# Performance work log

Hardware: AMD Instinct MI355X
Metric: run time of the kernel (lower is better)

## Reference

```python
import jax, jax.numpy as jnp
import numpy as np

IN_F = 4096
OUT_F = 4096
R = 16
LORA_ALPHA = 32
SCALING = LORA_ALPHA / R  # 2.0


def setup_inputs() -> dict:
    key = jax.random.key(0)
    k_x, k_w, k_b, k_a, k_bb = jax.random.split(key, 5)
    x = jax.random.normal(k_x, (4, 2048, IN_F), dtype=jnp.float32)
    # Simulate _quantize_4bit: build a float weight, quantize per-row to int4.
    w = jax.random.normal(k_w, (OUT_F, IN_F), dtype=jnp.float32) * 0.02
    max_abs = jnp.clip(jnp.max(jnp.abs(w), axis=1, keepdims=True), 1e-8, None)
    qscale = max_abs / 7.0                                   # [OUT_F, 1] float32
    qweight = jnp.clip(jnp.round(w / qscale), -8, 7).astype(jnp.int32)  # [OUT_F, IN_F]
    bias = jax.random.normal(k_b, (OUT_F,), dtype=jnp.float32) * 0.01
    # LoRA: A kaiming-uniform-like, B random (zeros init would make the LoRA path trivially zero).
    bound = 1.0 / np.sqrt(IN_F)
    lora_A = jax.random.uniform(k_a, (R, IN_F), minval=-bound, maxval=bound, dtype=jnp.float32)
    lora_B = jax.random.normal(k_bb, (OUT_F, R), dtype=jnp.float32) * 0.01
    return {"x": x, "qweight": qweight, "qscale": qscale, "bias": bias,
            "lora_A": lora_A, "lora_B": lora_B}


def reference(x, qweight, qscale, bias, lora_A, lora_B):
    # Dequantize int4 weights with per-row scale: W[o, i] = q[o, i] * s[o]
    W = qweight.astype(x.dtype) * qscale.astype(x.dtype)     # [OUT_F, IN_F]
    base = jnp.einsum('bsi,oi->bso', x, W) + bias            # F.linear(x, W, bias)
    # LoRA low-rank path (dropout=0 -> identity)
    lora = jnp.einsum('bsr,or->bso', jnp.einsum('bsi,ri->bsr', x, lora_A), lora_B)
    return base + lora * SCALING
```

## Files before the change

kernel.cpp:

```cpp
#include <hip/hip_runtime.h>
#include <hip/hip_bf16.h>
#include <stdint.h>


#define IN_F 4096
#define OUT_F 4096

typedef unsigned short u16;
typedef __attribute__((ext_vector_type(8))) short s16x8;
typedef __attribute__((ext_vector_type(4))) float f32x4;

__device__ inline u16 f2bf(float f) {
    union { float f; uint32_t u; } v; v.f = f;
    uint32_t u = v.u;
    return (u16)((u + 0x7FFFu + ((u >> 16) & 1u)) >> 16);
}

__global__ __launch_bounds__(256) void cvt_x_kernel(const float* __restrict__ x,
                                                    u16* __restrict__ xb, int n8) {
    int t = blockIdx.x * 256 + threadIdx.x;
    if (t >= n8) return;
    const float4* src = (const float4*)x + (size_t)t * 2;
    float4 a = src[0], b = src[1];
    union { u16 u[8]; s16x8 v; } o;
    o.u[0] = f2bf(a.x); o.u[1] = f2bf(a.y); o.u[2] = f2bf(a.z); o.u[3] = f2bf(a.w);
    o.u[4] = f2bf(b.x); o.u[5] = f2bf(b.y); o.u[6] = f2bf(b.z); o.u[7] = f2bf(b.w);
    ((s16x8*)xb)[t] = o.v;
}

__global__ __launch_bounds__(256) void build_weff_kernel(const int* __restrict__ qw,
                                                         const float* __restrict__ qs,
                                                         const float* __restrict__ lA,
                                                         const float* __restrict__ lB,
                                                         u16* __restrict__ w) {
    int t = blockIdx.x * 256 + threadIdx.x;
    int o  = t >> 9;
    int i0 = (t & 511) << 3;
    float s = qs[o];
    const int4* q4 = (const int4*)(qw + (size_t)o * IN_F + i0);
    int4 qa = q4[0], qb = q4[1];
    float acc[8];
    acc[0] = qa.x * s; acc[1] = qa.y * s; acc[2] = qa.z * s; acc[3] = qa.w * s;
    acc[4] = qb.x * s; acc[5] = qb.y * s; acc[6] = qb.z * s; acc[7] = qb.w * s;
#pragma unroll
    for (int r = 0; r < 16; ++r) {
        float br = 2.0f * lB[o * 16 + r];
        const float4* a4 = (const float4*)(lA + (size_t)r * IN_F + i0);
        float4 aa = a4[0], ab = a4[1];
        acc[0] += br * aa.x; acc[1] += br * aa.y; acc[2] += br * aa.z; acc[3] += br * aa.w;
        acc[4] += br * ab.x; acc[5] += br * ab.y; acc[6] += br * ab.z; acc[7] += br * ab.w;
    }
    union { u16 u[8]; s16x8 v; } ov;
#pragma unroll
    for (int j = 0; j < 8; ++j) ov.u[j] = f2bf(acc[j]);
    ((s16x8*)w)[t] = ov.v;
}

#define BK 32
#define NT (IN_F / BK)

#define GLD16(gp, lp)                                                          \
    __builtin_amdgcn_global_load_lds(                                          \
        (const __attribute__((address_space(1))) void*)(gp),                   \
        (__attribute__((address_space(3))) void*)(lp), 16, 0, 0)

__global__ __launch_bounds__(512, 2) void gemm_bt_kernel(const short* __restrict__ Xb,
                                                         const short* __restrict__ Wb,
                                                         const float* __restrict__ bias,
                                                         float* __restrict__ out,
                                                         int nmt) {
    __shared__ __align__(16) char smem[131072];

    const int tid  = threadIdx.x;
    const int w    = tid >> 6, lane = tid & 63;
    const int wm   = w >> 2, wn = w & 3;
    const int rl   = lane & 15;

    const int nwg = nmt * 16;
    const int cpx = nwg >> 3;
    const int f   = blockIdx.x;
    const int swz = (f & 7) * cpx + (f >> 3);
    const int m0  = (swz >> 4) * 256;
    const int n0  = (swz & 15) * 256;

    const int L0   = w * 1024 + lane * 16;
    const int S0   = L0 ^ (((lane >> 3) & 3) << 4);
    const int srow = S0 >> 6;
    const int scol = (S0 & 63) >> 1;
    const short* pA = Xb + (size_t)(m0 + srow) * IN_F + scol;
    const short* pB = Wb + (size_t)(n0 + srow) * IN_F + scol;
    char* ldsA = (char*)smem;
    char* ldsB = (char*)smem + 65536;
    const int woff = w * 1024;

#define STAGE_A(t) do { int bo_ = ((t) & 3) * 16384 + woff;                    \
        const short* s_ = pA + (size_t)(t) * BK;                               \
        GLD16(s_, ldsA + bo_);                                                 \
        GLD16(s_ + (size_t)128 * IN_F, ldsA + bo_ + 8192); } while (0)
#define STAGE_B(t) do { int bo_ = ((t) & 3) * 16384 + woff;                    \
        const short* s_ = pB + (size_t)(t) * BK;                               \
        GLD16(s_, ldsB + bo_);                                                 \
        GLD16(s_ + (size_t)128 * IN_F, ldsB + bo_ + 8192); } while (0)

    const int colpart = ((lane >> 4) * 16) ^ (((rl >> 1) & 3) << 4);
    const int aRow = (wm * 128 + rl) * 64 + colpart;
    const int bRow = (wn * 64 + rl) * 64 + colpart;

    f32x4 acc[8][4];
    f32x4 zero = {0.f, 0.f, 0.f, 0.f};
#pragma unroll
    for (int i = 0; i < 8; ++i)
#pragma unroll
        for (int j = 0; j < 4; ++j) acc[i][j] = zero;

    STAGE_A(0); STAGE_B(0); STAGE_A(1); STAGE_B(1); STAGE_A(2); STAGE_B(2);
    asm volatile("s_waitcnt vmcnt(8)" ::: "memory");
    __builtin_amdgcn_s_barrier();

    for (int t = 0; t < NT; ++t) {
        const char* aB = ldsA + (t & 3) * 16384 + aRow;
        const char* bB = ldsB + (t & 3) * 16384 + bRow;
        s16x8 a[8], b0, b1, b2, b3;

#pragma unroll
        for (int mi = 0; mi < 8; ++mi) a[mi] = *(const s16x8*)(aB + mi * 1024);
        b0 = *(const s16x8*)(bB);
        b1 = *(const s16x8*)(bB + 1024);
        if (t < NT - 3) STAGE_A(t + 3);
        __builtin_amdgcn_s_barrier();
        __builtin_amdgcn_s_setprio(1);
#pragma unroll
        for (int mi = 0; mi < 8; ++mi) {
            acc[mi][0] = __builtin_amdgcn_mfma_f32_16x16x32_bf16(a[mi], b0, acc[mi][0], 0, 0, 0);
            acc[mi][1] = __builtin_amdgcn_mfma_f32_16x16x32_bf16(a[mi], b1, acc[mi][1], 0, 0, 0);
        }
        __builtin_amdgcn_s_setprio(0);
        __builtin_amdgcn_s_barrier();

        b2 = *(const s16x8*)(bB + 2048);
        b3 = *(const s16x8*)(bB + 3072);
        if (t < NT - 3) STAGE_B(t + 3);
        __builtin_amdgcn_s_barrier();
        __builtin_amdgcn_s_setprio(1);
#pragma unroll
        for (int mi = 0; mi < 8; ++mi) {
            acc[mi][2] = __builtin_amdgcn_mfma_f32_16x16x32_bf16(a[mi], b2, acc[mi][2], 0, 0, 0);
            acc[mi][3] = __builtin_amdgcn_mfma_f32_16x16x32_bf16(a[mi], b3, acc[mi][3], 0, 0, 0);
        }
        __builtin_amdgcn_s_setprio(0);
        if (t <= NT - 4)      asm volatile("s_waitcnt vmcnt(8)" ::: "memory");
        else if (t == NT - 3) asm volatile("s_waitcnt vmcnt(4)" ::: "memory");
        else                  asm volatile("s_waitcnt vmcnt(0)" ::: "memory");
        __builtin_amdgcn_s_barrier();
    }

    const int rq = (lane >> 4) * 4;
#pragma unroll
    for (int ni = 0; ni < 4; ++ni) {
        int gn = n0 + wn * 64 + ni * 16 + rl;
        float bv = bias[gn];
#pragma unroll
        for (int mi = 0; mi < 8; ++mi) {
            int gm = m0 + wm * 128 + mi * 16 + rq;
#pragma unroll
            for (int r = 0; r < 4; ++r)
                out[(size_t)(gm + r) * OUT_F + gn] = acc[mi][ni][r] + bv;
        }
    }
#undef STAGE_A
#undef STAGE_B
}

extern "C" void kernel_launch(void* const* d_in, const int* in_sizes, int n_in,
                              void* d_out, int out_size, void* d_ws, size_t ws_size,
                              hipStream_t stream) {
    const float* x    = (const float*)d_in[0];
    const int*   qw   = (const int*)d_in[1];
    const float* qs   = (const float*)d_in[2];
    const float* bias = (const float*)d_in[3];
    const float* lA   = (const float*)d_in[4];
    const float* lB   = (const float*)d_in[5];
    float* out = (float*)d_out;

    const int xN = in_sizes[0];
    const int M  = xN / IN_F;
    const int nmt = M / 256;

    short* xb = (short*)d_ws;
    short* wb = xb + (size_t)xN;

    const int n8 = xN / 8;
    hipLaunchKernelGGL(cvt_x_kernel, dim3(n8 / 256), dim3(256), 0, stream,
                       x, (u16*)xb, n8);
    hipLaunchKernelGGL(build_weff_kernel, dim3((OUT_F * (IN_F / 8)) / 256), dim3(256),
                       0, stream, qw, qs, lA, lB, (u16*)wb);
    hipLaunchKernelGGL(gemm_bt_kernel, dim3(nmt * 16), dim3(512), 0, stream,
                       xb, wb, bias, out, nmt);
}
```

Before: 568.3 us.

## Compute LoRA as separate low-rank path instead of folding into weights

Stops folding 2*B@A into the dequantized bf16 weight. Instead it computes t1 = x@A^T in a small MFMA kernel and adds t1@(2B)^T in the main GEMM epilogue through shared memory. The x, weight and A conversions are merged into one prep launch, which removes the 16-rank accumulation loop from weight building. The cost is an extra pass over the bf16 activations and a small epilogue MFMA step, and the LoRA term is now computed from bf16 t1.

```diff
diff --git a/kernel.cpp b/kernel.cpp
--- a/kernel.cpp
+++ b/kernel.cpp
@@ -16,44 +16,72 @@
     return (u16)((u + 0x7FFFu + ((u >> 16) & 1u)) >> 16);
 }
 
-__global__ __launch_bounds__(256) void cvt_x_kernel(const float* __restrict__ x,
-                                                    u16* __restrict__ xb, int n8) {
-    int t = blockIdx.x * 256 + threadIdx.x;
-    if (t >= n8) return;
-    const float4* src = (const float4*)x + (size_t)t * 2;
-    float4 a = src[0], b = src[1];
-    union { u16 u[8]; s16x8 v; } o;
-    o.u[0] = f2bf(a.x); o.u[1] = f2bf(a.y); o.u[2] = f2bf(a.z); o.u[3] = f2bf(a.w);
-    o.u[4] = f2bf(b.x); o.u[5] = f2bf(b.y); o.u[6] = f2bf(b.z); o.u[7] = f2bf(b.w);
-    ((s16x8*)xb)[t] = o.v;
-}
-
-__global__ __launch_bounds__(256) void build_weff_kernel(const int* __restrict__ qw,
-                                                         const float* __restrict__ qs,
-                                                         const float* __restrict__ lA,
-                                                         const float* __restrict__ lB,
-                                                         u16* __restrict__ w) {
-    int t = blockIdx.x * 256 + threadIdx.x;
-    int o  = t >> 9;
-    int i0 = (t & 511) << 3;
-    float s = qs[o];
-    const int4* q4 = (const int4*)(qw + (size_t)o * IN_F + i0);
-    int4 qa = q4[0], qb = q4[1];
-    float acc[8];
-    acc[0] = qa.x * s; acc[1] = qa.y * s; acc[2] = qa.z * s; acc[3] = qa.w * s;
-    acc[4] = qb.x * s; acc[5] = qb.y * s; acc[6] = qb.z * s; acc[7] = qb.w * s;
-#pragma unroll
-    for (int r = 0; r < 16; ++r) {
-        float br = 2.0f * lB[o * 16 + r];
-        const float4* a4 = (const float4*)(lA + (size_t)r * IN_F + i0);
-        float4 aa = a4[0], ab = a4[1];
-        acc[0] += br * aa.x; acc[1] += br * aa.y; acc[2] += br * aa.z; acc[3] += br * aa.w;
-        acc[4] += br * ab.x; acc[5] += br * ab.y; acc[6] += br * ab.z; acc[7] += br * ab.w;
-    }
-    union { u16 u[8]; s16x8 v; } ov;
-#pragma unroll
-    for (int j = 0; j < 8; ++j) ov.u[j] = f2bf(acc[j]);
-    ((s16x8*)w)[t] = ov.v;
+__global__ __launch_bounds__(256) void prep_kernel(const float* __restrict__ x,
+                                                   const int* __restrict__ qw,
+                                                   const float* __restrict__ qs,
+                                                   const float* __restrict__ lA,
+                                                   u16* __restrict__ xb,
+                                                   u16* __restrict__ wb,
+                                                   u16* __restrict__ Ab,
+                                                   int nxblk) {
+    const int bid = blockIdx.x;
+    if (bid < nxblk) {
+        int t = bid * 256 + threadIdx.x;
+        const float4* src = (const float4*)x + (size_t)t * 2;
+        float4 a = src[0], b = src[1];
+        union { u16 u[8]; s16x8 v; } o;
+        o.u[0] = f2bf(a.x); o.u[1] = f2bf(a.y); o.u[2] = f2bf(a.z); o.u[3] = f2bf(a.w);
+        o.u[4] = f2bf(b.x); o.u[5] = f2bf(b.y); o.u[6] = f2bf(b.z); o.u[7] = f2bf(b.w);
+        ((s16x8*)xb)[t] = o.v;
+    } else if (bid < nxblk + 8192) {
+        int t = (bid - nxblk) * 256 + threadIdx.x;
+        int o = t >> 9, i0 = (t & 511) << 3;
+        float s = qs[o];
+        const int4* q4 = (const int4*)(qw + (size_t)o * IN_F + i0);
+        int4 qa = q4[0], qb = q4[1];
+        union { u16 u[8]; s16x8 v; } ov;
+        ov.u[0] = f2bf(qa.x * s); ov.u[1] = f2bf(qa.y * s);
+        ov.u[2] = f2bf(qa.z * s); ov.u[3] = f2bf(qa.w * s);
+        ov.u[4] = f2bf(qb.x * s); ov.u[5] = f2bf(qb.y * s);
+        ov.u[6] = f2bf(qb.z * s); ov.u[7] = f2bf(qb.w * s);
+        ((s16x8*)wb)[t] = ov.v;
+    } else {
+        int t = (bid - nxblk - 8192) * 256 + threadIdx.x;
+        const float4* src = (const float4*)lA + (size_t)t * 2;
+        float4 a = src[0], b = src[1];
+        union { u16 u[8]; s16x8 v; } o;
+        o.u[0] = f2bf(a.x); o.u[1] = f2bf(a.y); o.u[2] = f2bf(a.z); o.u[3] = f2bf(a.w);
+        o.u[4] = f2bf(b.x); o.u[5] = f2bf(b.y); o.u[6] = f2bf(b.z); o.u[7] = f2bf(b.w);
+        ((s16x8*)Ab)[t] = o.v;
+    }
+}
+
+__global__ __launch_bounds__(256) void lora_t1_kernel(const short* __restrict__ xb,
+                                                      const short* __restrict__ Ab,
+                                                      u16* __restrict__ t1) {
+    __shared__ float red[4][16][16];
+    const int tid = threadIdx.x;
+    const int w = tid >> 6, lane = tid & 63;
+    const int m0 = blockIdx.x * 16;
+    const int rsel = lane & 15, koff = (lane >> 4) * 8;
+
+    f32x4 acc = {0.f, 0.f, 0.f, 0.f};
+    const short* pa = xb + (size_t)(m0 + rsel) * IN_F + koff;
+    const short* pb = Ab + (size_t)rsel * IN_F + koff;
+#pragma unroll 4
+    for (int kt = w * 1024; kt < (w + 1) * 1024; kt += 32) {
+        s16x8 a = *(const s16x8*)(pa + kt);
+        s16x8 b = *(const s16x8*)(pb + kt);
+        acc = __builtin_amdgcn_mfma_f32_16x16x32_bf16(a, b, acc, 0, 0, 0);
+    }
+#pragma unroll
+    for (int r = 0; r < 4; ++r) red[w][(lane >> 4) * 4 + r][lane & 15] = acc[r];
+    __syncthreads();
+    if (tid < 256) {
+        int mr = tid >> 4, c = tid & 15;
+        float s = red[0][mr][c] + red[1][mr][c] + red[2][mr][c] + red[3][mr][c];
+        t1[(size_t)(m0 + mr) * 16 + c] = f2bf(s);
+    }
 }
 
 #define BK 32
@@ -67,6 +95,8 @@
 __global__ __launch_bounds__(512, 2) void gemm_bt_kernel(const short* __restrict__ Xb,
                                                          const short* __restrict__ Wb,
                                                          const float* __restrict__ bias,
+                                                         const short* __restrict__ t1,
+                                                         const float* __restrict__ lB,
                                                          float* __restrict__ out,
                                                          int nmt) {
     __shared__ __align__(16) char smem[131072];
@@ -152,6 +182,49 @@
         else if (t == NT - 3) asm volatile("s_waitcnt vmcnt(4)" ::: "memory");
         else                  asm volatile("s_waitcnt vmcnt(0)" ::: "memory");
         __builtin_amdgcn_s_barrier();
+    }
+
+    __syncthreads();
+    short* t1b = (short*)smem;
+    short* lbb = (short*)smem + 10240;
+    {
+        const int4 z4 = {0, 0, 0, 0};
+        if (tid < 256) {
+            const int4* src = (const int4*)(t1 + (size_t)(m0 + tid) * 16);
+            int4 v0 = src[0], v1 = src[1];
+            int4* dst = (int4*)&t1b[tid * 40];
+            dst[0] = v0; dst[1] = v1; dst[2] = z4; dst[3] = z4;
+        } else {
+            int r = tid - 256;
+            const float4* src = (const float4*)(lB + (size_t)(n0 + r) * 16);
+            float4 b0 = src[0], b1 = src[1], b2 = src[2], b3 = src[3];
+            union { u16 u[16]; int4 v[2]; } p;
+            p.u[0]  = f2bf(2.f * b0.x); p.u[1]  = f2bf(2.f * b0.y);
+            p.u[2]  = f2bf(2.f * b0.z); p.u[3]  = f2bf(2.f * b0.w);
+            p.u[4]  = f2bf(2.f * b1.x); p.u[5]  = f2bf(2.f * b1.y);
+            p.u[6]  = f2bf(2.f * b1.z); p.u[7]  = f2bf(2.f * b1.w);
+            p.u[8]  = f2bf(2.f * b2.x); p.u[9]  = f2bf(2.f * b2.y);
+            p.u[10] = f2bf(2.f * b2.z); p.u[11] = f2bf(2.f * b2.w);
+            p.u[12] = f2bf(2.f * b3.x); p.u[13] = f2bf(2.f * b3.y);
+            p.u[14] = f2bf(2.f * b3.z); p.u[15] = f2bf(2.f * b3.w);
+            int4* dst = (int4*)&lbb[r * 40];
+            dst[0] = p.v[0]; dst[1] = p.v[1]; dst[2] = z4; dst[3] = z4;
+        }
+    }
+    __syncthreads();
+    {
+        const int kb = (lane >> 4) * 16;
+        s16x8 bf2[4];
+#pragma unroll
+        for (int ni = 0; ni < 4; ++ni)
+            bf2[ni] = *(const s16x8*)((const char*)lbb + (wn * 64 + ni * 16 + rl) * 80 + kb);
+#pragma unroll
+        for (int mi = 0; mi < 8; ++mi) {
+            s16x8 af2 = *(const s16x8*)((const char*)t1b + (wm * 128 + mi * 16 + rl) * 80 + kb);
+#pragma unroll
+            for (int ni = 0; ni < 4; ++ni)
+                acc[mi][ni] = __builtin_amdgcn_mfma_f32_16x16x32_bf16(af2, bf2[ni], acc[mi][ni], 0, 0, 0);
+        }
     }
 
     const int rq = (lane >> 4) * 4;
@@ -188,12 +261,14 @@
 
     short* xb = (short*)d_ws;
     short* wb = xb + (size_t)xN;
-
-    const int n8 = xN / 8;
-    hipLaunchKernelGGL(cvt_x_kernel, dim3(n8 / 256), dim3(256), 0, stream,
-                       x, (u16*)xb, n8);
-    hipLaunchKernelGGL(build_weff_kernel, dim3((OUT_F * (IN_F / 8)) / 256), dim3(256),
-                       0, stream, qw, qs, lA, lB, (u16*)wb);
+    short* Ab = wb + (size_t)OUT_F * IN_F;
+    short* t1 = Ab + (size_t)16 * IN_F;
+
+    const int nxblk = xN / 8 / 256;
+    hipLaunchKernelGGL(prep_kernel, dim3(nxblk + 8192 + 32), dim3(256), 0, stream,
+                       x, qw, qs, lA, (u16*)xb, (u16*)wb, (u16*)Ab, nxblk);
+    hipLaunchKernelGGL(lora_t1_kernel, dim3(M / 16), dim3(256), 0, stream,
+                       xb, Ab, (u16*)t1);
     hipLaunchKernelGGL(gemm_bt_kernel, dim3(nmt * 16), dim3(512), 0, stream,
-                       xb, wb, bias, out, nmt);
-}
+                       xb, wb, bias, t1, lB, out, nmt);
+}
```

Result: faster. 527.6 us (-7.2%).
